# Kernel tuning notes

Hardware: AMD Instinct MI355X
Metric: run time of the kernel (lower is better)

Reference implementation:

```python
import jax, jax.numpy as jnp
import numpy as np

B, N, C, L = 2, 128, 256, 3
NODE_IN, EDGE_IN = 128, 64
KN, KE = 101, 7
ALPHA = 0.2
EPS = 1e-5

def lrelu(x):
    return jax.nn.leaky_relu(x, ALPHA)

def layer_norm(x, g, b):
    mu = jnp.mean(x, axis=-1, keepdims=True)
    var = jnp.mean((x - mu) ** 2, axis=-1, keepdims=True)
    return (x - mu) / jnp.sqrt(var + EPS) * g + b

def setup_inputs() -> dict:
    key = jax.random.key(0)
    ks = jax.random.split(key, 20)
    s = 0.05
    nodes = jax.random.normal(ks[0], (B, N, NODE_IN), jnp.float32)
    edges = jax.random.normal(ks[1], (B, N, N, EDGE_IN), jnp.float32)
    m = (jax.random.uniform(ks[2], (B, N, N)) > 0.3).astype(jnp.float32)
    adj_mask = jnp.maximum(m, jnp.eye(N, dtype=jnp.float32)[None])  # guarantee non-empty rows
    return {
        'nodes': nodes, 'edges': edges, 'adj_mask': adj_mask,
        'pnW': jax.random.normal(ks[3], (C, NODE_IN)) * s, 'pnb': jnp.zeros((C,)),
        'peW': jax.random.normal(ks[4], (C, EDGE_IN)) * s, 'peb': jnp.zeros((C,)),
        'Wb': jax.random.normal(ks[5], (L, C, 3 * C)) * s,
        'Wbp': jax.random.normal(ks[6], (L, C, C)) * s,
        'Wfp': jax.random.normal(ks[7], (L, C, C)) * s,
        'ub': jax.random.normal(ks[8], (L, C)) * s,
        'Wf': jax.random.normal(ks[9], (L, C, C)) * s,
        'eln_g': jnp.ones((L, C)), 'eln_b': jnp.zeros((L, C)),
        'nln_g': jnp.ones((L, C)), 'nln_b': jnp.zeros((L, C)),
        'ncW': jax.random.normal(ks[10], (KN, C)) * s, 'ncb': jnp.zeros((KN,)),
        'ecW': jax.random.normal(ks[11], (KE, C)) * s, 'ecb': jnp.zeros((KE,)),
    }

def reference(nodes, edges, adj_mask, pnW, pnb, peW, peb, Wb, Wbp, Wfp, ub, Wf,
              eln_g, eln_b, nln_g, nln_b, ncW, ncb, ecW, ecb):
    nodes = nodes @ pnW.T + pnb          # (B,N,C)
    edges = edges @ peW.T + peb          # (B,N,N,C)
    mask3 = adj_mask[..., None]
    for l in range(Wb.shape[0]):
        Cd = nodes.shape[-1]
        Wb1, Wb2, Wb3 = Wb[l][:, :Cd], Wb[l][:, Cd:2 * Cd], Wb[l][:, 2 * Cd:]
        # W_b([f_i, edges, f_j]) without materializing the (B,N,N,3C) concat
        ai = nodes @ Wb1.T                # (B,N,C) broadcast along j
        aj = nodes @ Wb3.T                # (B,N,C) broadcast along i
        ne = lrelu(ai[:, :, None, :] + edges @ Wb2.T + aj[:, None, :, :])
        ne = ne * mask3
        new_edges = layer_norm(ne + edges, eln_g[l], eln_b[l])
        edges_in = jnp.swapaxes(new_edges, 1, 2)      # permute(0,2,1,3)
        tn = nodes @ Wfp[l].T             # shared by term_node_i / term_node_j
        st = edges_in @ Wbp[l].T + tn[:, :, None, :] + tn[:, None, :, :]
        r = lrelu(st @ ub[l])             # (B,N,N)
        r = jnp.where(adj_mask > 0, r, -jnp.inf)
        attn = jnp.nan_to_num(jax.nn.softmax(r, axis=2))
        agg = jnp.einsum('bij,bjd->bid', attn, nodes @ Wf[l].T)
        nodes = layer_norm(lrelu(agg) + nodes, nln_g[l], nln_b[l])
        edges = new_edges
    node_logits = nodes @ ncW.T + ncb
    edge_logits = edges @ ecW.T + ecb
    return (nodes, edges, node_logits, edge_logits)
```

## Files before the change

kernel.cpp:

```cpp
#include <hip/hip_runtime.h>
#include <hip/hip_bf16.h>


#define ALPHA 0.2f
#define EPS_ 1e-5f

typedef __hip_bfloat16 bf16;
typedef __bf16 bf16x8 __attribute__((ext_vector_type(8)));
typedef __bf16 bf16x4 __attribute__((ext_vector_type(4)));
typedef float floatx4 __attribute__((ext_vector_type(4)));

__device__ __forceinline__ float bf2f(bf16 x){ return __bfloat162float(x); }
__device__ __forceinline__ bf16  f2bf(float x){ return __float2bfloat16(x); }
__device__ __forceinline__ float lrelu_f(float x){ return x > 0.f ? x : ALPHA * x; }

#define T_NODES 0u
#define T_EDGES 32768u
#define T_ADJ   2129920u
#define T_PNW   2162688u
#define T_PNB   2195456u
#define T_PEW   2195712u
#define T_PEB   2212096u
#define T_WB    2212352u
#define T_WBP   2802176u
#define T_WFP   2998784u
#define T_UB    3195392u
#define T_WF    3196160u
#define T_ELNG  3392768u
#define T_ELNB  3393536u
#define T_NLNG  3394304u
#define T_NLNB  3395072u
#define T_NCW   3395840u
#define T_NCB   3421696u
#define T_ECW   3421800u
#define T_ECB   3423592u

#define O_NODES 0u
#define O_EDGES 65536u
#define O_NLOG  8454144u
#define O_ELOG  8480000u

struct SrcPtrs { const void* p[20]; };

__device__ __forceinline__ float rawld(const void* p, size_t i, bool isb){
    return isb ? bf2f(((const bf16*)p)[i]) : ((const float*)p)[i];
}

__device__ __forceinline__ bf16x8 ldfrag8(const void* p, size_t e, bool isb){
    if (isb) return *reinterpret_cast<const bf16x8*>((const bf16*)p + e);
    const float4* f = (const float4*)((const float*)p + e);
    float4 a = f[0], b = f[1];
    bf16 o[8];
    o[0]=f2bf(a.x); o[1]=f2bf(a.y); o[2]=f2bf(a.z); o[3]=f2bf(a.w);
    o[4]=f2bf(b.x); o[5]=f2bf(b.y); o[6]=f2bf(b.z); o[7]=f2bf(b.w);
    return *reinterpret_cast<bf16x8*>(o);
}

__global__ __launch_bounds__(256) void setup_k(SrcPtrs sp, bf16* __restrict__ canon,
                                               float* __restrict__ vbuf, float* __restrict__ wbuf,
                                               float* __restrict__ nodes_cur,
                                               bf16* __restrict__ rw2, bf16* __restrict__ rpe){
    const unsigned short* probe = (const unsigned short*)sp.p[12];
    const bool isb = (probe[0] == 0x3F80);
    int blk = blockIdx.x, tid = threadIdx.x;
    int wave = tid >> 6, lane = tid & 63, quad = lane >> 4, l16 = lane & 15;

    if (blk < 1024){
        const unsigned COFF[20] = {T_NODES,T_EDGES,T_ADJ,T_PNW,T_PNB,T_PEW,T_PEB,T_WB,T_WBP,T_WFP,
                                   T_UB,T_WF,T_ELNG,T_ELNB,T_NLNG,T_NLNB,T_NCW,T_NCB,T_ECW,T_ECB};
        const unsigned SZ[20]   = {32768u,2097152u,32768u,32768u,256u,16384u,256u,589824u,196608u,196608u,
                                   768u,196608u,768u,768u,768u,768u,25856u,101u,1792u,7u};
        unsigned gtid = blk*256u + tid;
        unsigned gstride = 1024u*256u;
        for (int t = 0; t < 20; ++t){
            const void* src = sp.p[t];
            unsigned coff = COFF[t], n = SZ[t];
            unsigned chunks = n >> 3;
            if (isb){
                const uint4* s4 = (const uint4*)src;
                for (unsigned idx = gtid; idx < chunks; idx += gstride)
                    *reinterpret_cast<uint4*>(canon + coff + idx*8u) = s4[idx];
            } else {
                const float4* s4 = (const float4*)src;
                for (unsigned idx = gtid; idx < chunks; idx += gstride){
                    float4 a = s4[2*idx], b = s4[2*idx+1];
                    bf16 o[8];
                    o[0]=f2bf(a.x); o[1]=f2bf(a.y); o[2]=f2bf(a.z); o[3]=f2bf(a.w);
                    o[4]=f2bf(b.x); o[5]=f2bf(b.y); o[6]=f2bf(b.z); o[7]=f2bf(b.w);
                    *reinterpret_cast<uint4*>(canon + coff + idx*8u) = *reinterpret_cast<uint4*>(o);
                }
            }
            unsigned tail = n & 7u;
            if (gtid < tail){
                unsigned li = chunks*8u + gtid;
                canon[coff + li] = isb ? ((const bf16*)src)[li] : f2bf(((const float*)src)[li]);
            }
        }
    } else if (blk < 1030){
        int q = blk - 1024;
        int l = q >> 1, m = q & 1;
        const void* W = m ? sp.p[9] : sp.p[8];
        float* out = (m ? wbuf : vbuf) + l*256;
        int c = tid;
        __shared__ float shu[256];
        shu[c] = rawld(sp.p[10], l*256 + c, isb);
        __syncthreads();
        float a0=0.f, a1=0.f, a2=0.f, a3=0.f;
        for (int cp0 = 0; cp0 < 256; cp0 += 16){
#pragma unroll
            for (int j = 0; j < 16; ++j){
                float wv = rawld(W, (size_t)l*65536u + (size_t)(cp0+j)*256u + c, isb);
                float pr = shu[cp0+j] * wv;
                if ((j & 3) == 0) a0 += pr;
                else if ((j & 3) == 1) a1 += pr;
                else if ((j & 3) == 2) a2 += pr;
                else a3 += pr;
            }
        }
        out[c] = (a0 + a1) + (a2 + a3);
    } else if (blk < 1038){
        int row0 = (blk - 1030) * 32;
        floatx4 acc[2][4] = {};
#pragma unroll
        for (int k0c = 0; k0c < 4; ++k0c){
            int k0 = k0c*32;
            bf16x8 a[2], bb[4];
#pragma unroll
            for (int mt = 0; mt < 2; ++mt)
                a[mt] = ldfrag8(sp.p[0], (size_t)(row0 + mt*16 + l16)*128u + k0 + quad*8, isb);
#pragma unroll
            for (int nt = 0; nt < 4; ++nt)
                bb[nt] = ldfrag8(sp.p[3], (size_t)(wave*64 + nt*16 + l16)*128u + k0 + quad*8, isb);
#pragma unroll
            for (int mt = 0; mt < 2; ++mt)
#pragma unroll
                for (int nt = 0; nt < 4; ++nt)
                    acc[mt][nt] = __builtin_amdgcn_mfma_f32_16x16x32_bf16(a[mt], bb[nt], acc[mt][nt], 0, 0, 0);
        }
#pragma unroll
        for (int nt = 0; nt < 4; ++nt){
            int n = wave*64 + nt*16 + l16;
            float bn = rawld(sp.p[4], n, isb);
#pragma unroll
            for (int mt = 0; mt < 2; ++mt)
#pragma unroll
                for (int reg = 0; reg < 4; ++reg){
                    int r = row0 + mt*16 + quad*4 + reg;
                    nodes_cur[r*256 + n] = acc[mt][nt][reg] + bn;
                }
        }
    } else if (blk < 1086){
        int rb = blk - 1038;
        int l = rb >> 4, n_tile = rb & 15;
        bf16* dst = rw2 + l*65536;
#pragma unroll
        for (int half = 0; half < 2; ++half){
            int slot = half*256 + tid;
            int k0c = slot >> 6, ln = slot & 63;
            int qd = ln >> 4, lw = ln & 15;
            int n = n_tile*16 + lw;
            bf16 o[8];
#pragma unroll
            for (int j = 0; j < 8; ++j){
                int k = k0c*32 + qd*8 + j;
                o[j] = f2bf(rawld(sp.p[7], (size_t)l*196608u + (size_t)n*768u + 256u + k, isb));
            }
            *reinterpret_cast<uint4*>(dst + ((k0c*16 + n_tile)*64 + ln)*8) = *reinterpret_cast<uint4*>(o);
        }
    } else {
        int n_tile = blk - 1086;
        if (tid < 128){
            int slot = tid;
            int k0c = slot >> 6, ln = slot & 63;
            int qd = ln >> 4, lw = ln & 15;
            int n = n_tile*16 + lw;
            bf16 o[8];
#pragma unroll
            for (int j = 0; j < 8; ++j){
                int k = k0c*32 + qd*8 + j;
                o[j] = f2bf(rawld(sp.p[5], (size_t)n*64u + k, isb));
            }
            *reinterpret_cast<uint4*>(rpe + ((n_tile*2 + k0c)*64 + ln)*8) = *reinterpret_cast<uint4*>(o);
        }
    }
}

__global__ __launch_bounds__(512) void node_linears_k(
        const float* __restrict__ nodes_cur, const bf16* __restrict__ Wb_l,
        const bf16* __restrict__ Wf_l, const float* __restrict__ w_l,
        float* __restrict__ ai, float* __restrict__ aj,
        float* __restrict__ nf, float* __restrict__ s){
    int row = blockIdx.x;
    int tid = threadIdx.x;
    int wave = tid >> 6, lane = tid & 63;
    int c = tid & 255, kh = tid >> 8;
    __shared__ float x[256];
    __shared__ float red[8];
    __shared__ float pp1[2][256], pp3[2][256], ppf[2][256];

    if (tid < 256) x[c] = nodes_cur[row*256 + c];
    __syncthreads();
    if (tid < 256){
        float xs = x[c] * w_l[c];
        for (int off = 32; off; off >>= 1) xs += __shfl_xor(xs, off, 64);
        if (lane == 0) red[wave] = xs;
    }
    const bf16x8* w1 = reinterpret_cast<const bf16x8*>(Wb_l + (size_t)c*768 + kh*128);
    const bf16x8* w3 = reinterpret_cast<const bf16x8*>(Wb_l + (size_t)c*768 + 512 + kh*128);
    const bf16x8* wf = reinterpret_cast<const bf16x8*>(Wf_l + (size_t)c*256 + kh*128);
    const float* xb = x + kh*128;
    float a1 = 0.f, a3 = 0.f, f = 0.f;
#pragma unroll 4
    for (int ch = 0; ch < 16; ++ch){
        bf16x8 v1 = w1[ch], v3 = w3[ch], vf = wf[ch];
#pragma unroll
        for (int j = 0; j < 8; ++j){
            float xv = xb[ch*8 + j];
            a1 += xv * (float)v1[j];
            a3 += xv * (float)v3[j];
            f  += xv * (float)vf[j];
        }
    }
    pp1[kh][c] = a1; pp3[kh][c] = a3; ppf[kh][c] = f;
    __syncthreads();
    if (tid < 256){
        ai[row*256 + c] = pp1[0][c] + pp1[1][c];
        aj[row*256 + c] = pp3[0][c] + pp3[1][c];
        nf[row*256 + c] = ppf[0][c] + ppf[1][c];
    }
    if (tid == 0) s[row] = red[0] + red[1] + red[2] + red[3];
}

__global__ __launch_bounds__(256, 4) void edge_update2_k(
        bf16* __restrict__ Ebuf, const bf16* __restrict__ rw2_l,
        const float* __restrict__ ai, const float* __restrict__ aj,
        const bf16* __restrict__ adj, const bf16* __restrict__ g, const bf16* __restrict__ bta,
        const float* __restrict__ v, float* __restrict__ rbuf,
        int isfinal, const bf16* __restrict__ ecW, const bf16* __restrict__ ecb,
        void* __restrict__ dout, const unsigned short* __restrict__ probe,
        int isfirst, const bf16* __restrict__ eIn, const bf16* __restrict__ rpe,
        const bf16* __restrict__ peb){
    int row0 = blockIdx.x * 32;
    int b = row0 >> 14, i = (row0 >> 7) & 127, j0 = row0 & 127;
    int tid = threadIdx.x;
    int wave = tid >> 6, lane = tid & 63, quad = lane >> 4, l16 = lane & 15;

    __shared__ bf16  shA[32*264];
    __shared__ float sh_ai[256];
    __shared__ bf16  sh_w7b[7][256];
    __shared__ float smS[4][32];
    __shared__ float smQ[4][32];
    __shared__ float dvp[4][32];
    __shared__ float lgp[4][32][7];

    float maskv[2];
    float4 ajp[2][4];
#pragma unroll
    for (int rf = 0; rf < 2; ++rf){
        int j = j0 + rf*16 + l16;
        maskv[rf] = bf2f(adj[(b*128 + i)*128 + j]);
        const float* ajrow = aj + (size_t)(b*128 + j)*256 + wave*64;
#pragma unroll
        for (int mt = 0; mt < 4; ++mt)
            ajp[rf][mt] = *reinterpret_cast<const float4*>(ajrow + mt*16 + quad*4);
    }

    sh_ai[tid] = ai[(b*128 + i)*256 + tid];
    if (isfirst){
        floatx4 pacc[2][4] = {};
#pragma unroll
        for (int k0c = 0; k0c < 2; ++k0c){
            int k0 = k0c*32;
            bf16x8 a[2], bb[4];
#pragma unroll
            for (int mt = 0; mt < 2; ++mt)
                a[mt] = *reinterpret_cast<const bf16x8*>(eIn + (size_t)(row0 + mt*16 + l16)*64 + k0 + quad*8);
#pragma unroll
            for (int nt = 0; nt < 4; ++nt)
                bb[nt] = *reinterpret_cast<const bf16x8*>(rpe + ((size_t)((wave*4 + nt)*2 + k0c)*64 + lane)*8);
#pragma unroll
            for (int mt = 0; mt < 2; ++mt)
#pragma unroll
                for (int nt = 0; nt < 4; ++nt)
                    pacc[mt][nt] = __builtin_amdgcn_mfma_f32_16x16x32_bf16(a[mt], bb[nt], pacc[mt][nt], 0, 0, 0);
        }
#pragma unroll
        for (int nt = 0; nt < 4; ++nt){
            int col = wave*64 + nt*16 + l16;
            float bbv = bf2f(peb[col]);
#pragma unroll
            for (int mt = 0; mt < 2; ++mt)
#pragma unroll
                for (int reg = 0; reg < 4; ++reg)
                    shA[(mt*16 + quad*4 + reg)*264 + col] = f2bf(pacc[mt][nt][reg] + bbv);
        }
    } else {
#pragma unroll
        for (int it = 0; it < 4; ++it){
            int idx = it*256 + tid;
            int r = idx >> 5, c8 = idx & 31;
            bf16x8 vA = *reinterpret_cast<const bf16x8*>(Ebuf + (size_t)(row0 + r)*256 + c8*8);
            *reinterpret_cast<bf16x8*>(&shA[r*264 + c8*8]) = vA;
        }
    }
    if (isfinal){
        for (int idx = tid; idx < 7*256; idx += 256)
            sh_w7b[idx >> 8][idx & 255] = ecW[idx];
    }
    __syncthreads();

    floatx4 acc[4][2] = {};
    {
        const bf16* shb = &shA[l16*264];
#pragma unroll
        for (int k0c = 0; k0c < 8; ++k0c){
            bf16x8 bfr[2];
#pragma unroll
            for (int rf = 0; rf < 2; ++rf)
                bfr[rf] = *reinterpret_cast<const bf16x8*>(shb + rf*16*264 + k0c*32 + quad*8);
#pragma unroll
            for (int mt = 0; mt < 4; ++mt){
                bf16x8 afrag = *reinterpret_cast<const bf16x8*>(
                    rw2_l + ((size_t)(k0c*16 + wave*4 + mt)*64 + lane)*8);
#pragma unroll
                for (int rf = 0; rf < 2; ++rf)
                    acc[mt][rf] = __builtin_amdgcn_mfma_f32_16x16x32_bf16(afrag, bfr[rf], acc[mt][rf], 0, 0, 0);
            }
        }
    }

    const bool isb = (probe[0] == 0x3F80);
#pragma unroll
    for (int rf = 0; rf < 2; ++rf){
        int rl = rf*16 + l16;
        float sm = 0.f, q = 0.f;
#pragma unroll
        for (int mt = 0; mt < 4; ++mt){
            int c0 = wave*64 + mt*16 + quad*4;
            float4 aiv = *reinterpret_cast<const float4*>(sh_ai + c0);
            bf16x4 ev  = *reinterpret_cast<const bf16x4*>(&shA[rl*264 + c0]);
#pragma unroll
            for (int reg = 0; reg < 4; ++reg){
                float y = acc[mt][rf][reg] + ((const float*)&aiv)[reg] + ((const float*)&ajp[rf][mt])[reg];
                float x = lrelu_f(y) * maskv[rf] + (float)ev[reg];
                acc[mt][rf][reg] = x;
                sm += x; q += x*x;
            }
        }
        sm += __shfl_xor(sm, 16, 64); sm += __shfl_xor(sm, 32, 64);
        q  += __shfl_xor(q, 16, 64);  q  += __shfl_xor(q, 32, 64);
        if (quad == 0){ smS[wave][rl] = sm; smQ[wave][rl] = q; }
    }
    __syncthreads();

#pragma unroll
    for (int rf = 0; rf < 2; ++rf){
        int rl = rf*16 + l16;
        float ts = smS[0][rl] + smS[1][rl] + smS[2][rl] + smS[3][rl];
        float tq = smQ[0][rl] + smQ[1][rl] + smQ[2][rl] + smQ[3][rl];
        float mu  = ts * (1.f/256.f);
        float var = tq * (1.f/256.f) - mu*mu;
        float rstd = rsqrtf(var + EPS_);
        float dv = 0.f;
        float lg[7] = {0.f,0.f,0.f,0.f,0.f,0.f,0.f};
#pragma unroll
        for (int mt = 0; mt < 4; ++mt){
            int c0 = wave*64 + mt*16 + quad*4;
            bf16x4 gv4 = *reinterpret_cast<const bf16x4*>(g + c0);
            bf16x4 bv4 = *reinterpret_cast<const bf16x4*>(bta + c0);
            float4 vv  = *reinterpret_cast<const float4*>(v + c0);
            bf16x4 ob;
#pragma unroll
            for (int reg = 0; reg < 4; ++reg){
                float xo = (acc[mt][rf][reg] - mu) * rstd * (float)gv4[reg] + (float)bv4[reg];
                ob[reg] = f2bf(xo);
                dv += xo * ((const float*)&vv)[reg];
                if (isfinal){
#pragma unroll
                    for (int k = 0; k < 7; ++k) lg[k] += xo * (float)sh_w7b[k][c0 + reg];
                }
            }
            *reinterpret_cast<bf16x4*>(&shA[rl*264 + c0]) = ob;
        }
        dv += __shfl_xor(dv, 16, 64); dv += __shfl_xor(dv, 32, 64);
        if (quad == 0) dvp[wave][rl] = dv;
        if (isfinal){
#pragma unroll
            for (int k = 0; k < 7; ++k){
                lg[k] += __shfl_xor(lg[k], 16, 64);
                lg[k] += __shfl_xor(lg[k], 32, 64);
            }
            if (quad == 0){
#pragma unroll
                for (int k = 0; k < 7; ++k) lgp[wave][rl][k] = lg[k];
            }
        }
    }
    __syncthreads();

    if (!isfinal){
#pragma unroll
        for (int it = 0; it < 4; ++it){
            int idx = it*256 + tid;
            int r = idx >> 5, c8 = idx & 31;
            *reinterpret_cast<bf16x8*>(Ebuf + (size_t)(row0 + r)*256 + c8*8) =
                *reinterpret_cast<const bf16x8*>(&shA[r*264 + c8*8]);
        }
    } else if (isb){
#pragma unroll
        for (int it = 0; it < 4; ++it){
            int idx = it*256 + tid;
            int r = idx >> 5, c8 = idx & 31;
            *reinterpret_cast<bf16x8*>((bf16*)dout + O_EDGES + (size_t)(row0 + r)*256 + c8*8) =
                *reinterpret_cast<const bf16x8*>(&shA[r*264 + c8*8]);
        }
    } else {
#pragma unroll
        for (int it = 0; it < 4; ++it){
            int idx = it*256 + tid;
            int r = idx >> 5, c8 = idx & 31;
            bf16x8 vA = *reinterpret_cast<const bf16x8*>(&shA[r*264 + c8*8]);
            float4 f0, f1;
            f0.x = (float)vA[0]; f0.y = (float)vA[1]; f0.z = (float)vA[2]; f0.w = (float)vA[3];
            f1.x = (float)vA[4]; f1.y = (float)vA[5]; f1.z = (float)vA[6]; f1.w = (float)vA[7];
            float* op = (float*)dout + O_EDGES + (size_t)(row0 + r)*256 + c8*8;
            *reinterpret_cast<float4*>(op)     = f0;
            *reinterpret_cast<float4*>(op + 4) = f1;
        }
    }

    if (wave == 0 && quad == 0){
#pragma unroll
        for (int rf = 0; rf < 2; ++rf){
            int rl = rf*16 + l16;
            int j  = j0 + rl;
            int grow = row0 + rl;
            float d = dvp[0][rl] + dvp[1][rl] + dvp[2][rl] + dvp[3][rl];
            rbuf[(b*128 + j)*128 + i] = d;
            if (isfinal){
#pragma unroll
                for (int k = 0; k < 7; ++k){
                    float val = lgp[0][rl][k] + lgp[1][rl][k] + lgp[2][rl][k] + lgp[3][rl][k] + bf2f(ecb[k]);
                    if (isb) ((bf16*)dout)[O_ELOG + (size_t)grow*7 + k] = f2bf(val);
                    else     ((float*)dout)[O_ELOG + (size_t)grow*7 + k] = val;
                }
            }
        }
    }
}

__global__ __launch_bounds__(512) void node_update_k(
        const float* __restrict__ rbuf, const float* __restrict__ s_in, const bf16* __restrict__ adj,
        const float* __restrict__ nf_in, float* __restrict__ nodes_cur,
        const bf16* __restrict__ g, const bf16* __restrict__ bta,
        int isfinal,
        const bf16* __restrict__ Wb_nx, const bf16* __restrict__ Wf_nx, const float* __restrict__ w_nx,
        float* __restrict__ ai_o, float* __restrict__ aj_o, float* __restrict__ nf_o, float* __restrict__ s_o,
        const bf16* __restrict__ ncW, const bf16* __restrict__ ncb,
        void* __restrict__ dout, const unsigned short* __restrict__ probe){
    int row = blockIdx.x;
    int b = row >> 7;
    int tid = threadIdx.x;
    int wave = tid >> 6, lane = tid & 63;
    int c = tid & 255, kh = tid >> 8;
    __shared__ float attn[128];
    __shared__ float shr[32];
    __shared__ float shfx[256];
    __shared__ float aggp[2][256];
    __shared__ float pp1[2][256], pp3[2][256], ppf[2][256];

    float rv = -__builtin_inff();
    if (tid < 128){
        float t = rbuf[row*128 + tid] + s_in[row] + s_in[b*128 + tid];
        t = lrelu_f(t);
        rv = (bf2f(adj[row*128 + tid]) > 0.f) ? t : -__builtin_inff();
    }
    float m = rv;
    for (int off = 32; off; off >>= 1) m = fmaxf(m, __shfl_xor(m, off, 64));
    if (lane == 0 && wave < 2) shr[wave] = m;
    __syncthreads();
    float mx = fmaxf(shr[0], shr[1]);
    float e = (tid < 128 && rv > -__builtin_inff()) ? expf(rv - mx) : 0.f;
    if (tid < 128) attn[tid] = e;
    float se = e;
    for (int off = 32; off; off >>= 1) se += __shfl_xor(se, off, 64);
    if (lane == 0 && wave < 2) shr[2 + wave] = se;
    __syncthreads();
    float inv = 1.f / (shr[2] + shr[3]);

    {
        const float* nfb = nf_in + (size_t)b*32768 + c;
        int jb = kh*64;
        float g0 = 0.f, g1 = 0.f, g2 = 0.f, g3 = 0.f;
        float g4 = 0.f, g5 = 0.f, g6 = 0.f, g7 = 0.f;
        for (int jj = jb; jj < jb + 64; jj += 8){
            g0 += attn[jj]   * nfb[(size_t)jj*256];
            g1 += attn[jj+1] * nfb[(size_t)(jj+1)*256];
            g2 += attn[jj+2] * nfb[(size_t)(jj+2)*256];
            g3 += attn[jj+3] * nfb[(size_t)(jj+3)*256];
            g4 += attn[jj+4] * nfb[(size_t)(jj+4)*256];
            g5 += attn[jj+5] * nfb[(size_t)(jj+5)*256];
            g6 += attn[jj+6] * nfb[(size_t)(jj+6)*256];
            g7 += attn[jj+7] * nfb[(size_t)(jj+7)*256];
        }
        aggp[kh][c] = ((g0 + g1) + (g2 + g3)) + ((g4 + g5) + (g6 + g7));
    }
    __syncthreads();

    float x = 0.f;
    if (tid < 256){
        float agg = (aggp[0][c] + aggp[1][c]) * inv;
        x = lrelu_f(agg) + nodes_cur[row*256 + c];
        float xs = x, xq = x*x;
        for (int off = 32; off; off >>= 1){ xs += __shfl_xor(xs, off, 64); xq += __shfl_xor(xq, off, 64); }
        if (lane == 0){ shr[8 + wave] = xs; shr[16 + wave] = xq; }
    }
    __syncthreads();
    float out = 0.f;
    if (tid < 256){
        float sum = shr[8] + shr[9] + shr[10] + shr[11];
        float sq  = shr[16] + shr[17] + shr[18] + shr[19];
        float mu  = sum * (1.f/256.f);
        float var = sq * (1.f/256.f) - mu*mu;
        float rstd = rsqrtf(var + EPS_);
        out = (x - mu) * rstd * bf2f(g[c]) + bf2f(bta[c]);
        nodes_cur[row*256 + c] = out;
        shfx[c] = out;
        if (!isfinal){
            float ws2 = out * w_nx[c];
            for (int off = 32; off; off >>= 1) ws2 += __shfl_xor(ws2, off, 64);
            if (lane == 0) shr[24 + wave] = ws2;
        }
    }
    __syncthreads();

    if (!isfinal){
        const bf16x8* w1 = reinterpret_cast<const bf16x8*>(Wb_nx + (size_t)c*768 + kh*128);
        const bf16x8* w3 = reinterpret_cast<const bf16x8*>(Wb_nx + (size_t)c*768 + 512 + kh*128);
        const bf16x8* wf = reinterpret_cast<const bf16x8*>(Wf_nx + (size_t)c*256 + kh*128);
        const float* xb = shfx + kh*128;
        float a1 = 0.f, a3 = 0.f, f = 0.f;
#pragma unroll 4
        for (int ch = 0; ch < 16; ++ch){
            bf16x8 v1 = w1[ch], v3 = w3[ch], vf = wf[ch];
#pragma unroll
            for (int j = 0; j < 8; ++j){
                float xv = xb[ch*8 + j];
                a1 += xv * (float)v1[j];
                a3 += xv * (float)v3[j];
                f  += xv * (float)vf[j];
            }
        }
        pp1[kh][c] = a1; pp3[kh][c] = a3; ppf[kh][c] = f;
        __syncthreads();
        if (tid < 256){
            ai_o[row*256 + c] = pp1[0][c] + pp1[1][c];
            aj_o[row*256 + c] = pp3[0][c] + pp3[1][c];
            nf_o[row*256 + c] = ppf[0][c] + ppf[1][c];
        }
        if (tid == 0) s_o[row] = shr[24] + shr[25] + shr[26] + shr[27];
    } else {
        const bool isb = (probe[0] == 0x3F80);
        if (tid < 256){
            if (isb) ((bf16*)dout)[O_NODES + row*256 + c] = f2bf(out);
            else     ((float*)dout)[O_NODES + row*256 + c] = out;
        }
        if (c < 101){
            const bf16x8* wr = reinterpret_cast<const bf16x8*>(ncW + (size_t)c*256 + kh*128);
            const float* xb = shfx + kh*128;
            float acc = 0.f;
#pragma unroll 4
            for (int ch = 0; ch < 16; ++ch){
                bf16x8 wv = wr[ch];
#pragma unroll
                for (int j = 0; j < 8; ++j) acc += xb[ch*8 + j] * (float)wv[j];
            }
            pp1[kh][c] = acc;
        }
        __syncthreads();
        if (tid < 101){
            float val = pp1[0][tid] + pp1[1][tid] + bf2f(ncb[tid]);
            if (isb) ((bf16*)dout)[O_NLOG + row*101 + tid] = f2bf(val);
            else     ((float*)dout)[O_NLOG + row*101 + tid] = val;
        }
    }
}

extern "C" void kernel_launch(void* const* d_in, const int* in_sizes, int n_in,
                              void* d_out, int out_size, void* d_ws, size_t ws_size,
                              hipStream_t stream){
    (void)in_sizes; (void)n_in; (void)out_size; (void)ws_size;

    SrcPtrs sp;
    for (int i = 0; i < 20; ++i) sp.p[i] = d_in[i];
    const unsigned short* probe = (const unsigned short*)d_in[12];

    bf16* canon = (bf16*)d_ws;
    char* ws2 = (char*)d_ws + 6847488;
    bf16* Ebuf = (bf16*)ws2;
    float* f = (float*)(ws2 + 16777216);
    float* ai    = f;
    float* aj    = f + 65536;
    float* nfA   = f + 131072;
    float* nfB   = f + 196608;
    float* sA    = f + 262144;
    float* sB    = f + 262400;
    float* rbuf  = f + 262656;
    float* vbuf  = f + 295424;
    float* wbuf  = f + 296192;
    float* nodes_cur = f + 296960;
    bf16* rw2 = (bf16*)(f + 362496);
    bf16* rpe = rw2 + 196608;

    const bf16* c_edges = canon + T_EDGES;
    const bf16* c_adj   = canon + T_ADJ;
    const bf16* c_peb   = canon + T_PEB;
    const bf16* c_Wb    = canon + T_WB;
    const bf16* c_Wf    = canon + T_WF;
    const bf16* c_elng  = canon + T_ELNG;
    const bf16* c_elnb  = canon + T_ELNB;
    const bf16* c_nlng  = canon + T_NLNG;
    const bf16* c_nlnb  = canon + T_NLNB;
    const bf16* c_ncW   = canon + T_NCW;
    const bf16* c_ncb   = canon + T_NCB;
    const bf16* c_ecW   = canon + T_ECW;
    const bf16* c_ecb   = canon + T_ECB;

    setup_k<<<dim3(1102), dim3(256), 0, stream>>>(sp, canon, vbuf, wbuf, nodes_cur, rw2, rpe);
    node_linears_k<<<dim3(256), dim3(512), 0, stream>>>(
        nodes_cur, c_Wb, c_Wf, wbuf, ai, aj, nfA, sA);

    for (int l = 0; l < 3; ++l){
        int fin = (l == 2);
        int fst = (l == 0);
        float* nf_in = (l & 1) ? nfB : nfA;
        float* nf_out = (l & 1) ? nfA : nfB;
        float* s_in  = (l & 1) ? sB : sA;
        float* s_out = (l & 1) ? sA : sB;
        edge_update2_k<<<dim3(1024), dim3(256), 0, stream>>>(
            Ebuf, rw2 + l*65536, ai, aj, c_adj,
            c_elng + l*256, c_elnb + l*256, vbuf + l*256, rbuf,
            fin, c_ecW, c_ecb, d_out, probe,
            fst, c_edges, rpe, c_peb);
        node_update_k <<<dim3(256), dim3(512), 0, stream>>>(
            rbuf, s_in, c_adj, nf_in, nodes_cur, c_nlng + l*256, c_nlnb + l*256,
            fin,
            c_Wb + (size_t)(l+1)*196608, c_Wf + (size_t)(l+1)*65536, wbuf + (l+1)*256,
            ai, aj, nf_out, s_out,
            c_ncW, c_ncb, d_out, probe);
    }
}
```

Before: 256.1 us.

## Fold aj projection into edge-update MFMA via bf16 node tiles

```diff
diff --git a/kernel.cpp b/kernel.cpp
--- a/kernel.cpp
+++ b/kernel.cpp
@@ -58,8 +58,9 @@
 
 __global__ __launch_bounds__(256) void setup_k(SrcPtrs sp, bf16* __restrict__ canon,
                                                float* __restrict__ vbuf, float* __restrict__ wbuf,
-                                               float* __restrict__ nodes_cur,
-                                               bf16* __restrict__ rw2, bf16* __restrict__ rpe){
+                                               float* __restrict__ nodes_cur, bf16* __restrict__ nodes_bf,
+                                               bf16* __restrict__ rw2, bf16* __restrict__ rw3,
+                                               bf16* __restrict__ rpe){
     const unsigned short* probe = (const unsigned short*)sp.p[12];
     const bool isb = (probe[0] == 0x3F80);
     int blk = blockIdx.x, tid = threadIdx.x;
@@ -146,13 +147,18 @@
 #pragma unroll
                 for (int reg = 0; reg < 4; ++reg){
                     int r = row0 + mt*16 + quad*4 + reg;
-                    nodes_cur[r*256 + n] = acc[mt][nt][reg] + bn;
+                    float val = acc[mt][nt][reg] + bn;
+                    nodes_cur[r*256 + n] = val;
+                    nodes_bf[r*256 + n] = f2bf(val);
                 }
         }
-    } else if (blk < 1086){
+    } else if (blk < 1134){
         int rb = blk - 1038;
-        int l = rb >> 4, n_tile = rb & 15;
-        bf16* dst = rw2 + l*65536;
+        int which = rb >= 48;
+        int idx = which ? rb - 48 : rb;
+        int l = idx >> 4, n_tile = idx & 15;
+        bf16* dst = (which ? rw3 : rw2) + l*65536;
+        unsigned koff = which ? 512u : 256u;
 #pragma unroll
         for (int half = 0; half < 2; ++half){
             int slot = half*256 + tid;
@@ -163,12 +169,12 @@
 #pragma unroll
             for (int j = 0; j < 8; ++j){
                 int k = k0c*32 + qd*8 + j;
-                o[j] = f2bf(rawld(sp.p[7], (size_t)l*196608u + (size_t)n*768u + 256u + k, isb));
+                o[j] = f2bf(rawld(sp.p[7], (size_t)l*196608u + (size_t)n*768u + koff + k, isb));
             }
             *reinterpret_cast<uint4*>(dst + ((k0c*16 + n_tile)*64 + ln)*8) = *reinterpret_cast<uint4*>(o);
         }
     } else {
-        int n_tile = blk - 1086;
+        int n_tile = blk - 1134;
         if (tid < 128){
             int slot = tid;
             int k0c = slot >> 6, ln = slot & 63;
@@ -188,15 +194,14 @@
 __global__ __launch_bounds__(512) void node_linears_k(
         const float* __restrict__ nodes_cur, const bf16* __restrict__ Wb_l,
         const bf16* __restrict__ Wf_l, const float* __restrict__ w_l,
-        float* __restrict__ ai, float* __restrict__ aj,
-        float* __restrict__ nf, float* __restrict__ s){
+        float* __restrict__ ai, float* __restrict__ nf, float* __restrict__ s){
     int row = blockIdx.x;
     int tid = threadIdx.x;
     int wave = tid >> 6, lane = tid & 63;
     int c = tid & 255, kh = tid >> 8;
     __shared__ float x[256];
     __shared__ float red[8];
-    __shared__ float pp1[2][256], pp3[2][256], ppf[2][256];
+    __shared__ float pp1[2][256], ppf[2][256];
 
     if (tid < 256) x[c] = nodes_cur[row*256 + c];
     __syncthreads();
@@ -206,34 +211,31 @@
         if (lane == 0) red[wave] = xs;
     }
     const bf16x8* w1 = reinterpret_cast<const bf16x8*>(Wb_l + (size_t)c*768 + kh*128);
-    const bf16x8* w3 = reinterpret_cast<const bf16x8*>(Wb_l + (size_t)c*768 + 512 + kh*128);
     const bf16x8* wf = reinterpret_cast<const bf16x8*>(Wf_l + (size_t)c*256 + kh*128);
     const float* xb = x + kh*128;
-    float a1 = 0.f, a3 = 0.f, f = 0.f;
+    float a1 = 0.f, f = 0.f;
 #pragma unroll 4
     for (int ch = 0; ch < 16; ++ch){
-        bf16x8 v1 = w1[ch], v3 = w3[ch], vf = wf[ch];
+        bf16x8 v1 = w1[ch], vf = wf[ch];
 #pragma unroll
         for (int j = 0; j < 8; ++j){
             float xv = xb[ch*8 + j];
             a1 += xv * (float)v1[j];
-            a3 += xv * (float)v3[j];
             f  += xv * (float)vf[j];
         }
     }
-    pp1[kh][c] = a1; pp3[kh][c] = a3; ppf[kh][c] = f;
+    pp1[kh][c] = a1; ppf[kh][c] = f;
     __syncthreads();
     if (tid < 256){
         ai[row*256 + c] = pp1[0][c] + pp1[1][c];
-        aj[row*256 + c] = pp3[0][c] + pp3[1][c];
         nf[row*256 + c] = ppf[0][c] + ppf[1][c];
     }
     if (tid == 0) s[row] = red[0] + red[1] + red[2] + red[3];
 }
 
 __global__ __launch_bounds__(256, 4) void edge_update2_k(
-        bf16* __restrict__ Ebuf, const bf16* __restrict__ rw2_l,
-        const float* __restrict__ ai, const float* __restrict__ aj,
+        bf16* __restrict__ Ebuf, const bf16* __restrict__ rw2_l, const bf16* __restrict__ rw3_l,
+        const float* __restrict__ ai, const bf16* __restrict__ nodes_bf,
         const bf16* __restrict__ adj, const bf16* __restrict__ g, const bf16* __restrict__ bta,
         const float* __restrict__ v, float* __restrict__ rbuf,
         int isfinal, const bf16* __restrict__ ecW, const bf16* __restrict__ ecb,
@@ -246,26 +248,30 @@
     int wave = tid >> 6, lane = tid & 63, quad = lane >> 4, l16 = lane & 15;
 
     __shared__ bf16  shA[32*264];
-    __shared__ float sh_ai[256];
+    __shared__ bf16  shN[32*264];
     __shared__ bf16  sh_w7b[7][256];
     __shared__ float smS[4][32];
     __shared__ float smQ[4][32];
     __shared__ float dvp[4][32];
-    __shared__ float lgp[4][32][7];
+    float (*lgp)[32][7] = reinterpret_cast<float(*)[32][7]>(shN);
 
     float maskv[2];
-    float4 ajp[2][4];
-#pragma unroll
-    for (int rf = 0; rf < 2; ++rf){
-        int j = j0 + rf*16 + l16;
-        maskv[rf] = bf2f(adj[(b*128 + i)*128 + j]);
-        const float* ajrow = aj + (size_t)(b*128 + j)*256 + wave*64;
-#pragma unroll
-        for (int mt = 0; mt < 4; ++mt)
-            ajp[rf][mt] = *reinterpret_cast<const float4*>(ajrow + mt*16 + quad*4);
-    }
-
-    sh_ai[tid] = ai[(b*128 + i)*256 + tid];
+#pragma unroll
+    for (int rf = 0; rf < 2; ++rf)
+        maskv[rf] = bf2f(adj[(b*128 + i)*128 + j0 + rf*16 + l16]);
+    float4 aip[4];
+#pragma unroll
+    for (int mt = 0; mt < 4; ++mt)
+        aip[mt] = *reinterpret_cast<const float4*>(ai + (size_t)(b*128 + i)*256 + wave*64 + mt*16 + quad*4);
+
+#pragma unroll
+    for (int it = 0; it < 4; ++it){
+        int idx = it*256 + tid;
+        int r = idx >> 5, c8 = idx & 31;
+        *reinterpret_cast<bf16x8*>(&shN[r*264 + c8*8]) =
+            *reinterpret_cast<const bf16x8*>(nodes_bf + (size_t)(b*128 + j0 + r)*256 + c8*8);
+    }
+
     if (isfirst){
         floatx4 pacc[2][4] = {};
 #pragma unroll
@@ -327,6 +333,22 @@
                     acc[mt][rf] = __builtin_amdgcn_mfma_f32_16x16x32_bf16(afrag, bfr[rf], acc[mt][rf], 0, 0, 0);
             }
         }
+        const bf16* shn = &shN[l16*264];
+#pragma unroll
+        for (int k0c = 0; k0c < 8; ++k0c){
+            bf16x8 bfr[2];
+#pragma unroll
+            for (int rf = 0; rf < 2; ++rf)
+                bfr[rf] = *reinterpret_cast<const bf16x8*>(shn + rf*16*264 + k0c*32 + quad*8);
+#pragma unroll
+            for (int mt = 0; mt < 4; ++mt){
+                bf16x8 afrag = *reinterpret_cast<const bf16x8*>(
+                    rw3_l + ((size_t)(k0c*16 + wave*4 + mt)*64 + lane)*8);
+#pragma unroll
+                for (int rf = 0; rf < 2; ++rf)
+                    acc[mt][rf] = __builtin_amdgcn_mfma_f32_16x16x32_bf16(afrag, bfr[rf], acc[mt][rf], 0, 0, 0);
+            }
+        }
     }
 
     const bool isb = (probe[0] == 0x3F80);
@@ -337,11 +359,10 @@
 #pragma unroll
         for (int mt = 0; mt < 4; ++mt){
             int c0 = wave*64 + mt*16 + quad*4;
-            float4 aiv = *reinterpret_cast<const float4*>(sh_ai + c0);
-            bf16x4 ev  = *reinterpret_cast<const bf16x4*>(&shA[rl*264 + c0]);
+            bf16x4 ev = *reinterpret_cast<const bf16x4*>(&shA[rl*264 + c0]);
 #pragma unroll
             for (int reg = 0; reg < 4; ++reg){
-                float y = acc[mt][rf][reg] + ((const float*)&aiv)[reg] + ((const float*)&ajp[rf][mt])[reg];
+                float y = acc[mt][rf][reg] + ((const float*)&aip[mt])[reg];
                 float x = lrelu_f(y) * maskv[rf] + (float)ev[reg];
                 acc[mt][rf][reg] = x;
                 sm += x; q += x*x;
@@ -451,11 +472,11 @@
 
 __global__ __launch_bounds__(512) void node_update_k(
         const float* __restrict__ rbuf, const float* __restrict__ s_in, const bf16* __restrict__ adj,
-        const float* __restrict__ nf_in, float* __restrict__ nodes_cur,
+        const float* __restrict__ nf_in, float* __restrict__ nodes_cur, bf16* __restrict__ nodes_bf,
         const bf16* __restrict__ g, const bf16* __restrict__ bta,
         int isfinal,
         const bf16* __restrict__ Wb_nx, const bf16* __restrict__ Wf_nx, const float* __restrict__ w_nx,
-        float* __restrict__ ai_o, float* __restrict__ aj_o, float* __restrict__ nf_o, float* __restrict__ s_o,
+        float* __restrict__ ai_o, float* __restrict__ nf_o, float* __restrict__ s_o,
         const bf16* __restrict__ ncW, const bf16* __restrict__ ncb,
         void* __restrict__ dout, const unsigned short* __restrict__ probe){
     int row = blockIdx.x;
@@ -467,7 +488,7 @@
     __shared__ float shr[32];
     __shared__ float shfx[256];
     __shared__ float aggp[2][256];
-    __shared__ float pp1[2][256], pp3[2][256], ppf[2][256];
+    __shared__ float pp1[2][256], ppf[2][256];
 
     float rv = -__builtin_inff();
     if (tid < 128){
@@ -527,6 +548,7 @@
         nodes_cur[row*256 + c] = out;
         shfx[c] = out;
         if (!isfinal){
+            nodes_bf[row*256 + c] = f2bf(out);
             float ws2 = out * w_nx[c];
             for (int off = 32; off; off >>= 1) ws2 += __shfl_xor(ws2, off, 64);
             if (lane == 0) shr[24 + wave] = ws2;
@@ -536,26 +558,23 @@
 
     if (!isfinal){
         const bf16x8* w1 = reinterpret_cast<const bf16x8*>(Wb_nx + (size_t)c*768 + kh*128);
-        const bf16x8* w3 = reinterpret_cast<const bf16x8*>(Wb_nx + (size_t)c*768 + 512 + kh*128);
         const bf16x8* wf = reinterpret_cast<const bf16x8*>(Wf_nx + (size_t)c*256 + kh*128);
         const float* xb = shfx + kh*128;
-        float a1 = 0.f, a3 = 0.f, f = 0.f;
+        float a1 = 0.f, f = 0.f;
 #pragma unroll 4
         for (int ch = 0; ch < 16; ++ch){
-            bf16x8 v1 = w1[ch], v3 = w3[ch], vf = wf[ch];
+            bf16x8 v1 = w1[ch], vf = wf[ch];
 #pragma unroll
             for (int j = 0; j < 8; ++j){
                 float xv = xb[ch*8 + j];
                 a1 += xv * (float)v1[j];
-                a3 += xv * (float)v3[j];
                 f  += xv * (float)vf[j];
             }
         }
-        pp1[kh][c] = a1; pp3[kh][c] = a3; ppf[kh][c] = f;
+        pp1[kh][c] = a1; ppf[kh][c] = f;
         __syncthreads();
         if (tid < 256){
             ai_o[row*256 + c] = pp1[0][c] + pp1[1][c];
-            aj_o[row*256 + c] = pp3[0][c] + pp3[1][c];
             nf_o[row*256 + c] = ppf[0][c] + ppf[1][c];
         }
         if (tid == 0) s_o[row] = shr[24] + shr[25] + shr[26] + shr[27];
@@ -600,7 +619,6 @@
     bf16* Ebuf = (bf16*)ws2;
     float* f = (float*)(ws2 + 16777216);
     float* ai    = f;
-    float* aj    = f + 65536;
     float* nfA   = f + 131072;
     float* nfB   = f + 196608;
     float* sA    = f + 262144;
@@ -610,7 +628,9 @@
     float* wbuf  = f + 296192;
     float* nodes_cur = f + 296960;
     bf16* rw2 = (bf16*)(f + 362496);
-    bf16* rpe = rw2 + 196608;
+    bf16* rw3 = rw2 + 196608;
+    bf16* rpe = rw3 + 196608;
+    bf16* nodes_bf = rpe + 16384;
 
     const bf16* c_edges = canon + T_EDGES;
     const bf16* c_adj   = canon + T_ADJ;
@@ -626,9 +646,9 @@
     const bf16* c_ecW   = canon + T_ECW;
     const bf16* c_ecb   = canon + T_ECB;
 
-    setup_k<<<dim3(1102), dim3(256), 0, stream>>>(sp, canon, vbuf, wbuf, nodes_cur, rw2, rpe);
+    setup_k<<<dim3(1150), dim3(256), 0, stream>>>(sp, canon, vbuf, wbuf, nodes_cur, nodes_bf, rw2, rw3, rpe);
     node_linears_k<<<dim3(256), dim3(512), 0, stream>>>(
-        nodes_cur, c_Wb, c_Wf, wbuf, ai, aj, nfA, sA);
+        nodes_cur, c_Wb, c_Wf, wbuf, ai, nfA, sA);
 
     for (int l = 0; l < 3; ++l){
         int fin = (l == 2);
@@ -638,15 +658,15 @@
         float* s_in  = (l & 1) ? sB : sA;
         float* s_out = (l & 1) ? sA : sB;
         edge_update2_k<<<dim3(1024), dim3(256), 0, stream>>>(
-            Ebuf, rw2 + l*65536, ai, aj, c_adj,
+            Ebuf, rw2 + l*65536, rw3 + l*65536, ai, nodes_bf, c_adj,
             c_elng + l*256, c_elnb + l*256, vbuf + l*256, rbuf,
             fin, c_ecW, c_ecb, d_out, probe,
             fst, c_edges, rpe, c_peb);
         node_update_k <<<dim3(256), dim3(512), 0, stream>>>(
-            rbuf, s_in, c_adj, nf_in, nodes_cur, c_nlng + l*256, c_nlnb + l*256,
+            rbuf, s_in, c_adj, nf_in, nodes_cur, nodes_bf, c_nlng + l*256, c_nlnb + l*256,
             fin,
             c_Wb + (size_t)(l+1)*196608, c_Wf + (size_t)(l+1)*65536, wbuf + (l+1)*256,
-            ai, aj, nf_out, s_out,
+            ai, nf_out, s_out,
             c_ncW, c_ncb, d_out, probe);
     }
 }
```

New measurement: 264.9 us. 3.4% more time.
